# Kernel tuning notes

Hardware: AMD Instinct MI355X
Metric: run time of the kernel (lower is better)

Reference implementation:

```python
import jax, jax.numpy as jnp
import numpy as np

B, S, D = 8, 2048, 256


def setup_inputs() -> dict:
    key = jax.random.key(0)
    kq, kk, kv, km = jax.random.split(key, 4)
    q = jax.random.normal(kq, (B, S, D), dtype=jnp.float32)
    k = jax.random.normal(kk, (B, S, D), dtype=jnp.float32)
    v = jax.random.normal(kv, (B, S, D), dtype=jnp.float32)
    mask = jax.random.randint(km, (B, S, S), 0, 2, dtype=jnp.int32)
    return {"q": q, "k": k, "v": v, "mask": mask}


def reference(q, k, v, mask):
    d_k = q.shape[-1]
    scale = 1.0 / jnp.sqrt(jnp.float32(d_k))
    # scores: [B, S, S]
    attn = jnp.einsum('bqd,bkd->bqk', q, k) * scale
    attn = jnp.where(mask == 0, jnp.float32(-1e9), attn)
    attn = jax.nn.softmax(attn, axis=-1)
    out = jnp.einsum('bqk,bkd->bqd', attn, v)
    return (out, attn)
```

## Files before the change

kernel.cpp:

```cpp
#include <hip/hip_runtime.h>

constexpr int B = 8, S = 2048, D = 256;
constexpr int TQ = 32;
constexpr float SCALE = 0.0625f;
constexpr int PSTRIDE = 2056;

typedef __attribute__((ext_vector_type(8))) short bf16x8;
typedef __attribute__((ext_vector_type(4))) float f32x4;

__device__ __forceinline__ short f2bf(float f) {
    union { float f; unsigned u; } c; c.f = f;
    unsigned u = c.u + 0x7fffu + ((c.u >> 16) & 1u);
    return (short)(u >> 16);
}

__global__ void conv_bf16(const float* __restrict__ in, short* __restrict__ out, int n4) {
    int i = blockIdx.x * blockDim.x + threadIdx.x;
    if (i < n4) {
        float4 v = ((const float4*)in)[i];
        short4 o; o.x = f2bf(v.x); o.y = f2bf(v.y); o.z = f2bf(v.z); o.w = f2bf(v.w);
        ((short4*)out)[i] = o;
    }
}

__global__ void transpose_v(const float* __restrict__ v, short* __restrict__ vt) {
    const int b = blockIdx.z;
    const int d0 = blockIdx.x * 64, k0 = blockIdx.y * 64;
    const int t = threadIdx.x;
    const int tr = t >> 4, tc = t & 15;
    __shared__ float tile[64][65];
    const float* vb = v + (size_t)b * S * D;
    #pragma unroll
    for (int r = 0; r < 4; ++r) {
        int key = r * 16 + tr;
        float4 x = *(const float4*)(vb + (size_t)(k0 + key) * D + d0 + tc * 4);
        tile[key][tc * 4 + 0] = x.x; tile[key][tc * 4 + 1] = x.y;
        tile[key][tc * 4 + 2] = x.z; tile[key][tc * 4 + 3] = x.w;
    }
    __syncthreads();
    short* vtb = vt + (size_t)b * D * S;
    #pragma unroll
    for (int r = 0; r < 4; ++r) {
        int d = r * 16 + tr;
        short4 o;
        o.x = f2bf(tile[tc * 4 + 0][d]); o.y = f2bf(tile[tc * 4 + 1][d]);
        o.z = f2bf(tile[tc * 4 + 2][d]); o.w = f2bf(tile[tc * 4 + 3][d]);
        *(short4*)(vtb + (size_t)(d0 + d) * S + k0 + tc * 4) = o;
    }
}

__global__ __launch_bounds__(512, 2) void attn_mfma(
    const short* __restrict__ qb, const short* __restrict__ kb,
    const short* __restrict__ vtb, const int* __restrict__ maskg,
    float* __restrict__ outg, float* __restrict__ attng)
{
    const int b = blockIdx.y;
    const int i0 = blockIdx.x * TQ;
    const int tid = threadIdx.x;
    const int wave = tid >> 6, lane = tid & 63;
    const int quad = lane >> 4, l16 = lane & 15;

    __shared__ short p_lds[TQ][PSTRIDE];
    __shared__ float red[8][TQ];

    bf16x8 aq[2][8];
    const short* qbase = qb + ((size_t)b * S + i0) * D;
    #pragma unroll
    for (int mt = 0; mt < 2; ++mt)
        #pragma unroll
        for (int ks = 0; ks < 8; ++ks)
            aq[mt][ks] = *(const bf16x8*)(qbase + (size_t)(mt * 16 + l16) * D + ks * 32 + quad * 8);

    f32x4 acc[2][16];
    #pragma unroll
    for (int mt = 0; mt < 2; ++mt)
        #pragma unroll
        for (int nt = 0; nt < 16; ++nt)
            acc[mt][nt] = f32x4{0.f, 0.f, 0.f, 0.f};

    const short* kbase = kb + (size_t)b * S * D;
    #pragma unroll
    for (int nt = 0; nt < 16; ++nt) {
        const int n0 = wave * 256 + nt * 16;
        bf16x8 bk[8];
        #pragma unroll
        for (int ks = 0; ks < 8; ++ks)
            bk[ks] = *(const bf16x8*)(kbase + (size_t)(n0 + l16) * D + ks * 32 + quad * 8);
        #pragma unroll
        for (int ks = 0; ks < 8; ++ks) {
            acc[0][nt] = __builtin_amdgcn_mfma_f32_16x16x32_bf16(aq[0][ks], bk[ks], acc[0][nt], 0, 0, 0);
            acc[1][nt] = __builtin_amdgcn_mfma_f32_16x16x32_bf16(aq[1][ks], bk[ks], acc[1][nt], 0, 0, 0);
        }
    }

    float rsum[2][4];
    #pragma unroll
    for (int mt = 0; mt < 2; ++mt)
        #pragma unroll
        for (int r = 0; r < 4; ++r) rsum[mt][r] = 0.f;

    #pragma unroll
    for (int mt = 0; mt < 2; ++mt) {
        const int* mbase = maskg + ((size_t)b * S + i0 + mt * 16 + quad * 4) * S;
        #pragma unroll
        for (int nt = 0; nt < 16; ++nt) {
            const int col = wave * 256 + nt * 16 + l16;
            #pragma unroll
            for (int r = 0; r < 4; ++r) {
                int m = mbase[(size_t)r * S + col];
                float s = (m == 0) ? -1e9f : acc[mt][nt][r] * SCALE;
                float e = __expf(s);
                acc[mt][nt][r] = e;
                rsum[mt][r] += e;
            }
        }
    }
    #pragma unroll
    for (int mt = 0; mt < 2; ++mt)
        #pragma unroll
        for (int r = 0; r < 4; ++r) {
            float v = rsum[mt][r];
            v += __shfl_xor(v, 1); v += __shfl_xor(v, 2);
            v += __shfl_xor(v, 4); v += __shfl_xor(v, 8);
            rsum[mt][r] = v;
            if (l16 == 0) red[wave][mt * 16 + quad * 4 + r] = v;
        }
    __syncthreads();

    float inv[2][4];
    #pragma unroll
    for (int mt = 0; mt < 2; ++mt)
        #pragma unroll
        for (int r = 0; r < 4; ++r) {
            float tot = 0.f;
            #pragma unroll
            for (int w = 0; w < 8; ++w) tot += red[w][mt * 16 + quad * 4 + r];
            inv[mt][r] = 1.0f / tot;
        }

    #pragma unroll
    for (int mt = 0; mt < 2; ++mt) {
        float* abase = attng + ((size_t)b * S + i0 + mt * 16 + quad * 4) * S;
        #pragma unroll
        for (int nt = 0; nt < 16; ++nt) {
            const int col = wave * 256 + nt * 16 + l16;
            #pragma unroll
            for (int r = 0; r < 4; ++r) {
                float p = acc[mt][nt][r] * inv[mt][r];
                abase[(size_t)r * S + col] = p;
                p_lds[mt * 16 + quad * 4 + r][col] = f2bf(p);
            }
        }
    }
    __syncthreads();

    f32x4 oacc[2][2];
    #pragma unroll
    for (int mt = 0; mt < 2; ++mt)
        #pragma unroll
        for (int nc = 0; nc < 2; ++nc) oacc[mt][nc] = f32x4{0.f, 0.f, 0.f, 0.f};

    const short* vbase = vtb + (size_t)b * D * S;
    const int nb = wave * 32;
    for (int ks = 0; ks < 64; ++ks) {
        bf16x8 ap[2], bv[2];
        #pragma unroll
        for (int mt = 0; mt < 2; ++mt)
            ap[mt] = *(const bf16x8*)&p_lds[mt * 16 + l16][ks * 32 + quad * 8];
        #pragma unroll
        for (int nc = 0; nc < 2; ++nc)
            bv[nc] = *(const bf16x8*)(vbase + (size_t)(nb + nc * 16 + l16) * S + ks * 32 + quad * 8);
        #pragma unroll
        for (int mt = 0; mt < 2; ++mt)
            #pragma unroll
            for (int nc = 0; nc < 2; ++nc)
                oacc[mt][nc] = __builtin_amdgcn_mfma_f32_16x16x32_bf16(ap[mt], bv[nc], oacc[mt][nc], 0, 0, 0);
    }

    #pragma unroll
    for (int mt = 0; mt < 2; ++mt)
        #pragma unroll
        for (int nc = 0; nc < 2; ++nc)
            #pragma unroll
            for (int r = 0; r < 4; ++r) {
                int row = i0 + mt * 16 + quad * 4 + r;
                int col = nb + nc * 16 + l16;
                outg[((size_t)b * S + row) * D + col] = oacc[mt][nc][r];
            }
}

extern "C" void kernel_launch(void* const* d_in, const int* in_sizes, int n_in,
                              void* d_out, int out_size, void* d_ws, size_t ws_size,
                              hipStream_t stream) {
    const float* q    = (const float*)d_in[0];
    const float* k    = (const float*)d_in[1];
    const float* v    = (const float*)d_in[2];
    const int*   mask = (const int*)d_in[3];
    float* out  = (float*)d_out;
    float* attn = out + (size_t)B * S * D;

    const size_t N = (size_t)B * S * D;
    short* qb  = (short*)d_ws;
    short* kb  = qb + N;
    short* vtb = kb + N;

    const int n4 = (int)(N / 4);
    conv_bf16<<<dim3(n4 / 256), 256, 0, stream>>>(q, qb, n4);
    conv_bf16<<<dim3(n4 / 256), 256, 0, stream>>>(k, kb, n4);
    transpose_v<<<dim3(D / 64, S / 64, B), 256, 0, stream>>>(v, vtb);

    attn_mfma<<<dim3(S / TQ, B), 512, 0, stream>>>(qb, kb, vtb, mask, out, attn);
}
```

Before: 413.6 us.

## Pack mask to bits, halve query tile, fuse Q conversion into attention kernel

Adds a pre-pass that packs the int32 mask into 64-bit ballot words, so the attention kernel reads bits instead of ints. The query tile drops from 32 to 16 rows and occupancy is raised to 4 blocks per CU. Q is now converted to bf16 inside the attention kernel, which removes one conversion launch, and the batch index is interleaved in the block id. Smaller tiles mean K and V are reread twice as often, and the separate mask-packing pass still reads the full int32 mask once.

```diff
diff --git a/kernel.cpp b/kernel.cpp
--- a/kernel.cpp
+++ b/kernel.cpp
@@ -1,7 +1,7 @@
 #include <hip/hip_runtime.h>
 
 constexpr int B = 8, S = 2048, D = 256;
-constexpr int TQ = 32;
+constexpr int TQ = 16;
 constexpr float SCALE = 0.0625f;
 constexpr int PSTRIDE = 2056;
 
@@ -49,13 +49,26 @@
     }
 }
 
-__global__ __launch_bounds__(512, 2) void attn_mfma(
-    const short* __restrict__ qb, const short* __restrict__ kb,
-    const short* __restrict__ vtb, const int* __restrict__ maskg,
+__global__ void pack_mask(const int* __restrict__ m, unsigned long long* __restrict__ pm) {
+    const int lane = threadIdx.x & 63;
+    const size_t wid = ((size_t)blockIdx.x * blockDim.x + threadIdx.x) >> 6;
+    const size_t base = wid * 256;
+    #pragma unroll
+    for (int i = 0; i < 4; ++i) {
+        int v = m[base + i * 64 + lane];
+        unsigned long long bal = __ballot(v != 0);
+        if (lane == 0) pm[(base >> 6) + i] = bal;
+    }
+}
+
+__global__ __launch_bounds__(512, 4) void attn_mfma(
+    const float* __restrict__ qg, const short* __restrict__ kb,
+    const short* __restrict__ vtb, const unsigned long long* __restrict__ pm,
     float* __restrict__ outg, float* __restrict__ attng)
 {
-    const int b = blockIdx.y;
-    const int i0 = blockIdx.x * TQ;
+    const int id = blockIdx.x;
+    const int b  = id & 7;
+    const int i0 = (id >> 3) * TQ;
     const int tid = threadIdx.x;
     const int wave = tid >> 6, lane = tid & 63;
     const int quad = lane >> 4, l16 = lane & 15;
@@ -63,130 +76,108 @@
     __shared__ short p_lds[TQ][PSTRIDE];
     __shared__ float red[8][TQ];
 
-    bf16x8 aq[2][8];
-    const short* qbase = qb + ((size_t)b * S + i0) * D;
-    #pragma unroll
-    for (int mt = 0; mt < 2; ++mt)
+    bf16x8 aq[8];
+    {
+        const float* qrow = qg + ((size_t)b * S + i0 + l16) * D + quad * 8;
+        #pragma unroll
+        for (int ks = 0; ks < 8; ++ks) {
+            float4 f0 = *(const float4*)(qrow + ks * 32);
+            float4 f1 = *(const float4*)(qrow + ks * 32 + 4);
+            bf16x8 t;
+            t[0] = f2bf(f0.x); t[1] = f2bf(f0.y); t[2] = f2bf(f0.z); t[3] = f2bf(f0.w);
+            t[4] = f2bf(f1.x); t[5] = f2bf(f1.y); t[6] = f2bf(f1.z); t[7] = f2bf(f1.w);
+            aq[ks] = t;
+        }
+    }
+
+    f32x4 acc[16];
+    #pragma unroll
+    for (int nt = 0; nt < 16; ++nt) acc[nt] = f32x4{0.f, 0.f, 0.f, 0.f};
+
+    const short* kbase = kb + (size_t)b * S * D;
+    #pragma unroll 4
+    for (int nt = 0; nt < 16; ++nt) {
+        const short* kr = kbase + (size_t)(wave * 256 + nt * 16 + l16) * D + quad * 8;
+        bf16x8 bk[8];
+        #pragma unroll
+        for (int ks = 0; ks < 8; ++ks) bk[ks] = *(const bf16x8*)(kr + ks * 32);
         #pragma unroll
         for (int ks = 0; ks < 8; ++ks)
-            aq[mt][ks] = *(const bf16x8*)(qbase + (size_t)(mt * 16 + l16) * D + ks * 32 + quad * 8);
-
-    f32x4 acc[2][16];
-    #pragma unroll
-    for (int mt = 0; mt < 2; ++mt)
-        #pragma unroll
-        for (int nt = 0; nt < 16; ++nt)
-            acc[mt][nt] = f32x4{0.f, 0.f, 0.f, 0.f};
-
-    const short* kbase = kb + (size_t)b * S * D;
-    #pragma unroll
-    for (int nt = 0; nt < 16; ++nt) {
-        const int n0 = wave * 256 + nt * 16;
-        bf16x8 bk[8];
-        #pragma unroll
-        for (int ks = 0; ks < 8; ++ks)
-            bk[ks] = *(const bf16x8*)(kbase + (size_t)(n0 + l16) * D + ks * 32 + quad * 8);
-        #pragma unroll
-        for (int ks = 0; ks < 8; ++ks) {
-            acc[0][nt] = __builtin_amdgcn_mfma_f32_16x16x32_bf16(aq[0][ks], bk[ks], acc[0][nt], 0, 0, 0);
-            acc[1][nt] = __builtin_amdgcn_mfma_f32_16x16x32_bf16(aq[1][ks], bk[ks], acc[1][nt], 0, 0, 0);
-        }
-    }
-
-    float rsum[2][4];
-    #pragma unroll
-    for (int mt = 0; mt < 2; ++mt)
-        #pragma unroll
-        for (int r = 0; r < 4; ++r) rsum[mt][r] = 0.f;
-
-    #pragma unroll
-    for (int mt = 0; mt < 2; ++mt) {
-        const int* mbase = maskg + ((size_t)b * S + i0 + mt * 16 + quad * 4) * S;
-        #pragma unroll
-        for (int nt = 0; nt < 16; ++nt) {
-            const int col = wave * 256 + nt * 16 + l16;
+            acc[nt] = __builtin_amdgcn_mfma_f32_16x16x32_bf16(aq[ks], bk[ks], acc[nt], 0, 0, 0);
+    }
+
+    float rsum[4] = {0.f, 0.f, 0.f, 0.f};
+    {
+        const unsigned long long* pmb = pm + ((size_t)b * S + i0 + quad * 4) * (S / 64) + wave * 4;
+        #pragma unroll
+        for (int g = 0; g < 4; ++g) {
+            unsigned long long mw[4];
             #pragma unroll
-            for (int r = 0; r < 4; ++r) {
-                int m = mbase[(size_t)r * S + col];
-                float s = (m == 0) ? -1e9f : acc[mt][nt][r] * SCALE;
-                float e = __expf(s);
-                acc[mt][nt][r] = e;
-                rsum[mt][r] += e;
+            for (int r = 0; r < 4; ++r) mw[r] = pmb[(size_t)r * (S / 64) + g];
+            #pragma unroll
+            for (int nt2 = 0; nt2 < 4; ++nt2) {
+                const int nt = g * 4 + nt2;
+                const int bitpos = nt2 * 16 + l16;
+                #pragma unroll
+                for (int r = 0; r < 4; ++r) {
+                    float e = ((mw[r] >> bitpos) & 1ull) ? __expf(acc[nt][r] * SCALE) : 0.f;
+                    acc[nt][r] = e;
+                    rsum[r] += e;
+                }
             }
         }
     }
     #pragma unroll
-    for (int mt = 0; mt < 2; ++mt)
+    for (int r = 0; r < 4; ++r) {
+        float v = rsum[r];
+        v += __shfl_xor(v, 1); v += __shfl_xor(v, 2);
+        v += __shfl_xor(v, 4); v += __shfl_xor(v, 8);
+        if (l16 == 0) red[wave][quad * 4 + r] = v;
+    }
+    __syncthreads();
+
+    float inv[4];
+    #pragma unroll
+    for (int r = 0; r < 4; ++r) {
+        const int row = quad * 4 + r;
+        float tot = 0.f;
+        #pragma unroll
+        for (int w = 0; w < 8; ++w) tot += red[w][row];
+        inv[r] = 1.0f / tot;
+    }
+
+    #pragma unroll 4
+    for (int nt = 0; nt < 16; ++nt) {
+        const int col = wave * 256 + nt * 16 + l16;
         #pragma unroll
         for (int r = 0; r < 4; ++r) {
-            float v = rsum[mt][r];
-            v += __shfl_xor(v, 1); v += __shfl_xor(v, 2);
-            v += __shfl_xor(v, 4); v += __shfl_xor(v, 8);
-            rsum[mt][r] = v;
-            if (l16 == 0) red[wave][mt * 16 + quad * 4 + r] = v;
+            float p = acc[nt][r] * inv[r];
+            attng[((size_t)b * S + i0 + quad * 4 + r) * S + col] = p;
+            p_lds[quad * 4 + r][col] = f2bf(p);
         }
+    }
     __syncthreads();
 
-    float inv[2][4];
-    #pragma unroll
-    for (int mt = 0; mt < 2; ++mt)
-        #pragma unroll
-        for (int r = 0; r < 4; ++r) {
-            float tot = 0.f;
-            #pragma unroll
-            for (int w = 0; w < 8; ++w) tot += red[w][mt * 16 + quad * 4 + r];
-            inv[mt][r] = 1.0f / tot;
-        }
-
-    #pragma unroll
-    for (int mt = 0; mt < 2; ++mt) {
-        float* abase = attng + ((size_t)b * S + i0 + mt * 16 + quad * 4) * S;
-        #pragma unroll
-        for (int nt = 0; nt < 16; ++nt) {
-            const int col = wave * 256 + nt * 16 + l16;
-            #pragma unroll
-            for (int r = 0; r < 4; ++r) {
-                float p = acc[mt][nt][r] * inv[mt][r];
-                abase[(size_t)r * S + col] = p;
-                p_lds[mt * 16 + quad * 4 + r][col] = f2bf(p);
-            }
-        }
-    }
-    __syncthreads();
-
-    f32x4 oacc[2][2];
-    #pragma unroll
-    for (int mt = 0; mt < 2; ++mt)
-        #pragma unroll
-        for (int nc = 0; nc < 2; ++nc) oacc[mt][nc] = f32x4{0.f, 0.f, 0.f, 0.f};
+    f32x4 oacc[2];
+    oacc[0] = f32x4{0.f, 0.f, 0.f, 0.f};
+    oacc[1] = f32x4{0.f, 0.f, 0.f, 0.f};
 
     const short* vbase = vtb + (size_t)b * D * S;
     const int nb = wave * 32;
+    #pragma unroll 2
     for (int ks = 0; ks < 64; ++ks) {
-        bf16x8 ap[2], bv[2];
-        #pragma unroll
-        for (int mt = 0; mt < 2; ++mt)
-            ap[mt] = *(const bf16x8*)&p_lds[mt * 16 + l16][ks * 32 + quad * 8];
-        #pragma unroll
-        for (int nc = 0; nc < 2; ++nc)
-            bv[nc] = *(const bf16x8*)(vbase + (size_t)(nb + nc * 16 + l16) * S + ks * 32 + quad * 8);
-        #pragma unroll
-        for (int mt = 0; mt < 2; ++mt)
-            #pragma unroll
-            for (int nc = 0; nc < 2; ++nc)
-                oacc[mt][nc] = __builtin_amdgcn_mfma_f32_16x16x32_bf16(ap[mt], bv[nc], oacc[mt][nc], 0, 0, 0);
-    }
-
-    #pragma unroll
-    for (int mt = 0; mt < 2; ++mt)
-        #pragma unroll
-        for (int nc = 0; nc < 2; ++nc)
-            #pragma unroll
-            for (int r = 0; r < 4; ++r) {
-                int row = i0 + mt * 16 + quad * 4 + r;
-                int col = nb + nc * 16 + l16;
-                outg[((size_t)b * S + row) * D + col] = oacc[mt][nc][r];
-            }
+        bf16x8 ap = *(const bf16x8*)&p_lds[l16][ks * 32 + quad * 8];
+        bf16x8 bv0 = *(const bf16x8*)(vbase + (size_t)(nb + l16) * S + ks * 32 + quad * 8);
+        bf16x8 bv1 = *(const bf16x8*)(vbase + (size_t)(nb + 16 + l16) * S + ks * 32 + quad * 8);
+        oacc[0] = __builtin_amdgcn_mfma_f32_16x16x32_bf16(ap, bv0, oacc[0], 0, 0, 0);
+        oacc[1] = __builtin_amdgcn_mfma_f32_16x16x32_bf16(ap, bv1, oacc[1], 0, 0, 0);
+    }
+
+    #pragma unroll
+    for (int nc = 0; nc < 2; ++nc)
+        #pragma unroll
+        for (int r = 0; r < 4; ++r)
+            outg[((size_t)b * S + i0 + quad * 4 + r) * D + nb + nc * 16 + l16] = oacc[nc][r];
 }
 
 extern "C" void kernel_launch(void* const* d_in, const int* in_sizes, int n_in,
@@ -200,14 +191,14 @@
     float* attn = out + (size_t)B * S * D;
 
     const size_t N = (size_t)B * S * D;
-    short* qb  = (short*)d_ws;
-    short* kb  = qb + N;
+    short* kb  = (short*)d_ws;
     short* vtb = kb + N;
+    unsigned long long* pm = (unsigned long long*)(vtb + N);
 
     const int n4 = (int)(N / 4);
-    conv_bf16<<<dim3(n4 / 256), 256, 0, stream>>>(q, qb, n4);
     conv_bf16<<<dim3(n4 / 256), 256, 0, stream>>>(k, kb, n4);
     transpose_v<<<dim3(D / 64, S / 64, B), 256, 0, stream>>>(v, vtb);
-
-    attn_mfma<<<dim3(S / TQ, B), 512, 0, stream>>>(qb, kb, vtb, mask, out, attn);
-}
+    pack_mask<<<dim3((B * S * (S / 64)) / (4 * 4)), 256, 0, stream>>>(mask, pm);
+
+    attn_mfma<<<dim3((S / TQ) * B), 512, 0, stream>>>(q, kb, vtb, pm, out, attn);
+}
```

Result: slower. 606.2 us (+46.5%).
